# Kernel tuning notes

Measured on AMD Instinct MI355X. Metric: run time of the kernel, lower is better.

The kernel has to match this reference:

```python
import jax, jax.numpy as jnp
import numpy as np

NUM_HEADS = 16
DIM_EMBED = 1024
DIM_CROSS = 768
DIM_HEAD = DIM_EMBED // NUM_HEADS


def setup_inputs() -> dict:
    key = jax.random.key(0)
    ks = jax.random.split(key, 10)
    B, Sq, Skv = 16, 4096, 77
    s_e = 1.0 / np.sqrt(DIM_EMBED)
    s_c = 1.0 / np.sqrt(DIM_CROSS)
    return {
        "x": jax.random.normal(ks[0], (B, Sq, DIM_EMBED), jnp.float32),
        "y": jax.random.normal(ks[1], (B, Skv, DIM_CROSS), jnp.float32),
        "wq": jax.random.uniform(ks[2], (DIM_EMBED, DIM_EMBED), jnp.float32, -s_e, s_e),
        "bq": jax.random.uniform(ks[3], (DIM_EMBED,), jnp.float32, -s_e, s_e),
        "wk": jax.random.uniform(ks[4], (DIM_CROSS, DIM_EMBED), jnp.float32, -s_c, s_c),
        "bk": jax.random.uniform(ks[5], (DIM_EMBED,), jnp.float32, -s_c, s_c),
        "wv": jax.random.uniform(ks[6], (DIM_CROSS, DIM_EMBED), jnp.float32, -s_c, s_c),
        "bv": jax.random.uniform(ks[7], (DIM_EMBED,), jnp.float32, -s_c, s_c),
        "wo": jax.random.uniform(ks[8], (DIM_EMBED, DIM_EMBED), jnp.float32, -s_e, s_e),
        "bo": jax.random.uniform(ks[9], (DIM_EMBED,), jnp.float32, -s_e, s_e),
    }


def reference(x, y, wq, bq, wk, bk, wv, bv, wo, bo):
    B, Sq, E = x.shape
    H, D = NUM_HEADS, DIM_HEAD
    q = (x @ wq + bq).reshape(B, Sq, H, D).transpose(0, 2, 1, 3)   # [B,H,Sq,D]
    k = (y @ wk + bk).reshape(B, -1, H, D).transpose(0, 2, 1, 3)   # [B,H,Skv,D]
    v = (y @ wv + bv).reshape(B, -1, H, D).transpose(0, 2, 1, 3)   # [B,H,Skv,D]
    scale = 1.0 / jnp.sqrt(jnp.asarray(D, dtype=q.dtype))
    scores = jnp.einsum("bhqd,bhkd->bhqk", q, k) * scale           # [B,H,Sq,Skv]
    attn = jax.nn.softmax(scores, axis=-1)
    out = jnp.einsum("bhqk,bhkd->bhqd", attn, v)                   # [B,H,Sq,D]
    out = out.transpose(0, 2, 1, 3).reshape(B, Sq, E)
    return out @ wo + bo
```

## Files before the change

### kernel.cpp

```cpp
#include <hip/hip_runtime.h>

typedef unsigned short u16;
typedef __attribute__((ext_vector_type(4))) float f32x4;
typedef __attribute__((ext_vector_type(8))) short bf16x8;
typedef __attribute__((ext_vector_type(8))) unsigned short u16x8;
typedef __attribute__((ext_vector_type(4))) unsigned short u16x4;

__device__ __forceinline__ u16 f2bf(float f) {
  union { float f; unsigned u; } v; v.f = f;
  unsigned r = v.u + 0x7FFFu + ((v.u >> 16) & 1u);
  return (u16)(r >> 16);
}
__device__ __forceinline__ float bf2f(u16 h) {
  union { unsigned u; float f; } v; v.u = ((unsigned)h) << 16; return v.f;
}

__device__ __forceinline__ void gload_lds16(const void* g, void* l) {
  __builtin_amdgcn_global_load_lds((const __attribute__((address_space(1))) void*)g,
                                   (__attribute__((address_space(3))) void*)l, 16, 0, 0);
}


__global__ void k_zero(u16x8* __restrict__ p, int n8) {
  int i = blockIdx.x * blockDim.x + threadIdx.x;
  int stride = gridDim.x * blockDim.x;
  u16x8 z = (u16x8)0;
  for (; i < n8; i += stride) p[i] = z;
}

__global__ void k_cvt_x(const float* __restrict__ in, u16* __restrict__ out, int n4) {
  int i = blockIdx.x * blockDim.x + threadIdx.x;
  int stride = gridDim.x * blockDim.x;
  const f32x4* in4 = (const f32x4*)in;
  u16x4* out4 = (u16x4*)out;
  for (; i < n4; i += stride) {
    f32x4 v = in4[i];
    u16x4 o;
    o[0] = f2bf(v[0]); o[1] = f2bf(v[1]); o[2] = f2bf(v[2]); o[3] = f2bf(v[3]);
    out4[i] = o;
  }
}

__global__ void k_prep_wt(const float* __restrict__ wq, const float* __restrict__ wo,
                          const float* __restrict__ wk, const float* __restrict__ wv,
                          u16* __restrict__ WQ1T, u16* __restrict__ WO1T,
                          u16* __restrict__ WK1T, u16* __restrict__ WV1T) {
  __shared__ u16 tile[64][72];
  int bid = blockIdx.x;
  const float* w; u16* o; int K;
  if (bid < 256)      { w = wq; o = WQ1T; K = 1024; }
  else if (bid < 512) { w = wo; o = WO1T; K = 1024; bid -= 256; }
  else if (bid < 704) { w = wk; o = WK1T; K = 768;  bid -= 512; }
  else                { w = wv; o = WV1T; K = 768;  bid -= 704; }
  const int ti = bid >> 4, tj = bid & 15;
  const int t = threadIdx.x;
  const int r = t >> 2, cq = (t & 3) * 16;

  const float* src = w + (size_t)(ti * 64 + r) * 1024 + tj * 64 + cq;
#pragma unroll
  for (int j4 = 0; j4 < 4; ++j4) {
    f32x4 v = *(const f32x4*)(src + j4 * 4);
#pragma unroll
    for (int e = 0; e < 4; ++e) tile[r][cq + j4 * 4 + e] = f2bf(v[e]);
  }
  __syncthreads();

  u16 vals[16];
#pragma unroll
  for (int j = 0; j < 16; ++j) vals[j] = tile[cq + j][r];
  u16* dst = o + (size_t)(tj * 64 + r) * K + ti * 64 + cq;
  *(u16x8*)dst = *(u16x8*)&vals[0];
  *(u16x8*)(dst + 8) = *(u16x8*)&vals[8];
}

__global__ void k_prep_y(const float* __restrict__ y, u16* __restrict__ yb, int n4) {
  int i = blockIdx.x * blockDim.x + threadIdx.x;
  int stride = gridDim.x * blockDim.x;
  const f32x4* in4 = (const f32x4*)y;
  u16x4* out4 = (u16x4*)yb;
  for (; i < n4; i += stride) {
    f32x4 v = in4[i];
    u16x4 o;
    o[0] = f2bf(v[0]); o[1] = f2bf(v[1]); o[2] = f2bf(v[2]); o[3] = f2bf(v[3]);
    out4[i] = o;
  }
}

__global__ __launch_bounds__(256, 2) void k_gemm_kv(
    const u16* __restrict__ A,
    const u16* __restrict__ BK1, const float* __restrict__ bkb, u16* __restrict__ KTo,
    const u16* __restrict__ BV1, const float* __restrict__ bvb, u16* __restrict__ VTo)
{
  const int M = 1232, Kdim = 768;
  __shared__ u16 sA[128 * 32];
  __shared__ u16 sB[128 * 32];
  const int t = threadIdx.x;
  const int half = blockIdx.x >= 80;
  const int bb = blockIdx.x - half * 80;
  const u16* B = half ? BV1 : BK1;
  const float* bias = half ? bvb : bkb;
  u16* outp = half ? VTo : KTo;
  const int bm = bb / 8, bn = bb % 8;
  const int m0 = bm * 128, n0 = bn * 128;
  const int l = t & 63, wv_ = t >> 6;
  const int lr = l & 15, lg = l >> 4;
  const int wm = (wv_ >> 1) * 64, wn = (wv_ & 1) * 64;

  const int srow = t >> 2;
  const int ssw = ((t >> 2) & 3) ^ ((t >> 4) & 3);
  const int scol = ((t & 3) ^ ssw) * 8;
  char* ldsA = (char*)sA;
  char* ldsB = (char*)sB;
  const int ldsoff = wv_ * 1024;

  const int swl = (lr & 3) ^ ((lr >> 2) & 3);
  const int rds = (lg ^ swl) * 8;

  f32x4 acc[4][4] = {};

  for (int kt = 0; kt < Kdim / 32; ++kt) {
    const int k0 = kt * 32;
    __syncthreads();
    {
      int r1 = m0 + srow;       if (r1 > M - 1) r1 = M - 1;
      int r2 = m0 + 64 + srow;  if (r2 > M - 1) r2 = M - 1;
      gload_lds16(A + (size_t)r1 * Kdim + k0 + scol, ldsA + 0    + ldsoff);
      gload_lds16(A + (size_t)r2 * Kdim + k0 + scol, ldsA + 4096 + ldsoff);
      gload_lds16(B + (size_t)(n0 + srow) * Kdim + k0 + scol,      ldsB + 0    + ldsoff);
      gload_lds16(B + (size_t)(n0 + 64 + srow) * Kdim + k0 + scol, ldsB + 4096 + ldsoff);
    }
    __syncthreads();
    bf16x8 af[4], bfr[4];
#pragma unroll
    for (int mt = 0; mt < 4; ++mt)
      af[mt] = *(const bf16x8*)&sA[(wm + mt * 16 + lr) * 32 + rds];
#pragma unroll
    for (int nt = 0; nt < 4; ++nt)
      bfr[nt] = *(const bf16x8*)&sB[(wn + nt * 16 + lr) * 32 + rds];
#pragma unroll
    for (int mt = 0; mt < 4; ++mt)
#pragma unroll
      for (int nt = 0; nt < 4; ++nt)
        acc[mt][nt] = __builtin_amdgcn_mfma_f32_16x16x32_bf16(af[mt], bfr[nt], acc[mt][nt], 0, 0, 0);
  }

#pragma unroll
  for (int mt = 0; mt < 4; ++mt) {
#pragma unroll
    for (int nt = 0; nt < 4; ++nt) {
      const int gc = n0 + wn + nt * 16 + lr;
      const float bb2 = bias[gc];
#pragma unroll
      for (int r = 0; r < 4; ++r) {
        const int gr = m0 + wm + mt * 16 + lg * 4 + r;
        const float v = acc[mt][nt][r] + bb2;
        if (gr < M) {
          int bI = gr / 77, s = gr - bI * 77;
          int hh = gc >> 6, d = gc & 63;
          if (!half)
            outp[(((size_t)bI * 16 + hh) * 96 + s) * 64 + d] = f2bf(v);
          else
            outp[(((size_t)bI * 16 + hh) * 64 + d) * 96 + s] = f2bf(v);
        }
      }
    }
  }
}

template <int EPI>
__global__ __launch_bounds__(512, 2) void gemm256(
    const u16* __restrict__ A, const u16* __restrict__ Bp,
    const float* __restrict__ bias, void* __restrict__ outp)
{
  __shared__ char lds[131072];
  const int t = threadIdx.x;
  const int cpx = (int)gridDim.x >> 3;
  const int swz = ((int)blockIdx.x & 7) * cpx + ((int)blockIdx.x >> 3);
  const int bm = swz >> 2, bn = swz & 3;
  const int m0 = bm * 256, n0 = bn * 256;
  const int w = t >> 6, l = t & 63, lr = l & 15, lg = l >> 4;
  const int wm = w >> 2, wn = w & 3;

  const int srow = t >> 2;
  const int scol = ((t & 3) ^ ((t >> 2) & 3) ^ ((t >> 4) & 3)) * 8;
  const int rsw = (lg ^ (lr & 3) ^ ((lr >> 2) & 3)) << 4;
  const int arow = wm * 128 + lr;
  const int brow = wn * 64 + lr;

  f32x4 acc[8][4] = {};

#define RD(dstA, dstB, sbb) { \
  _Pragma("unroll") for (int q = 0; q < 8; ++q) \
    dstA[q] = *(const bf16x8*)(lds + (sbb) + ((arow + q * 16) << 6) + rsw); \
  _Pragma("unroll") for (int nt = 0; nt < 4; ++nt) \
    dstB[nt] = *(const bf16x8*)(lds + (sbb) + 16384 + ((brow + nt * 16) << 6) + rsw); }
#define STAGE(kt, sbb) { \
    gload_lds16(A  + (size_t)(m0 + srow) * 1024 + (kt) * 32 + scol,       lds + (sbb) + t * 16); \
    gload_lds16(A  + (size_t)(m0 + 128 + srow) * 1024 + (kt) * 32 + scol, lds + (sbb) + 8192 + t * 16); \
    gload_lds16(Bp + (size_t)(n0 + srow) * 1024 + (kt) * 32 + scol,       lds + (sbb) + 16384 + t * 16); \
    gload_lds16(Bp + (size_t)(n0 + 128 + srow) * 1024 + (kt) * 32 + scol, lds + (sbb) + 24576 + t * 16); }
#define MM(a_, b_) { __builtin_amdgcn_s_setprio(1); \
  _Pragma("unroll") for (int q = 0; q < 8; ++q) \
    _Pragma("unroll") for (int nt = 0; nt < 4; ++nt) \
      acc[q][nt] = __builtin_amdgcn_mfma_f32_16x16x32_bf16(a_[q], b_[nt], acc[q][nt], 0, 0, 0); \
  __builtin_amdgcn_s_setprio(0); }
#define BAR __builtin_amdgcn_s_barrier()
#define SB0 __builtin_amdgcn_sched_barrier(0)
#define VM8 asm volatile("s_waitcnt vmcnt(8)" ::: "memory")

  bf16x8 aA[8], bA[4], aB[8], bB[4];

  STAGE(0, 0); STAGE(1, 32768); STAGE(2, 65536);
  VM8; SB0; BAR;
  RD(aA, bA, 0);

  int rdo = 32768, sto = 98304;
#pragma unroll 1
  for (int tt = 0; tt < 32; tt += 2) {
    {
      int ks = tt + 3; if (ks > 31) ks = 31;
      STAGE(ks, sto); sto = (sto + 32768) & 131071;
      VM8; SB0; BAR;
      RD(aB, bB, rdo); rdo = (rdo + 32768) & 131071;
      MM(aA, bA);
      BAR;
    }
    {
      int ks = tt + 4; if (ks > 31) ks = 31;
      STAGE(ks, sto); sto = (sto + 32768) & 131071;
      VM8; SB0; BAR;
      RD(aA, bA, rdo); rdo = (rdo + 32768) & 131071;
      MM(aB, bB);
      BAR;
    }
  }
  asm volatile("s_waitcnt vmcnt(0)" ::: "memory");
  SB0;

#undef RD
#undef STAGE
#undef MM
#undef BAR
#undef SB0
#undef VM8

#pragma unroll
  for (int q = 0; q < 8; ++q) {
#pragma unroll
    for (int nt = 0; nt < 4; ++nt) {
      const int gc = n0 + wn * 64 + nt * 16 + lr;
      const float bb = bias[gc];
#pragma unroll
      for (int r = 0; r < 4; ++r) {
        const int gr = m0 + wm * 128 + q * 16 + lg * 4 + r;
        const float v = acc[q][nt][r] + bb;
        if constexpr (EPI == 0) {
          ((u16*)outp)[(size_t)gr * 1024 + gc] = f2bf(v);
        } else {
          ((float*)outp)[(size_t)gr * 1024 + gc] = v;
        }
      }
    }
  }
}

__global__ __launch_bounds__(256) void k_attn(const u16* __restrict__ KT,
                                              const u16* __restrict__ VT,
                                              u16* __restrict__ QB)
{
  __shared__ u16 sK[96 * 72];
  __shared__ u16 sV[64 * 104];
  __shared__ u16 sP[4][32 * 104];

  const int bid = blockIdx.x;
  const int h = bid & 15, b = (bid >> 4) & 15, blk = bid >> 8;
  const int t = threadIdx.x;

  const u16* gK = KT + (size_t)(b * 16 + h) * (96 * 64);
  const u16* gV = VT + (size_t)(b * 16 + h) * (64 * 96);
#pragma unroll
  for (int c = 0; c < 3; ++c) {
    int e = t * 8 + c * 2048;
    { int row = e >> 6, col = e & 63;
      *(u16x8*)&sK[row * 72 + col] = *(const u16x8*)&gK[e]; }
    { int row = e / 96, col = e - (e / 96) * 96;
      *(u16x8*)&sV[row * 104 + col] = *(const u16x8*)&gV[e]; }
  }
  __syncthreads();

  const int l = t & 63, w = t >> 6, lr = l & 15, lg = l >> 4;
  const size_t rowbase = (size_t)b * 4096 + blk * 128 + w * 32;

  bf16x8 aq[2][2];
#pragma unroll
  for (int mt = 0; mt < 2; ++mt)
#pragma unroll
    for (int ks = 0; ks < 2; ++ks)
      aq[mt][ks] = *(const bf16x8*)&QB[(rowbase + mt * 16 + lr) * 1024 + h * 64 + ks * 32 + lg * 8];

  f32x4 s_[2][5] = {};
#pragma unroll
  for (int nt = 0; nt < 5; ++nt) {
#pragma unroll
    for (int ks = 0; ks < 2; ++ks) {
      bf16x8 bk = *(const bf16x8*)&sK[(nt * 16 + lr) * 72 + ks * 32 + lg * 8];
#pragma unroll
      for (int mt = 0; mt < 2; ++mt)
        s_[mt][nt] = __builtin_amdgcn_mfma_f32_16x16x32_bf16(aq[mt][ks], bk, s_[mt][nt], 0, 0, 0);
    }
  }
#pragma unroll
  for (int mt = 0; mt < 2; ++mt)
#pragma unroll
    for (int nt = 0; nt < 5; ++nt)
#pragma unroll
      for (int r = 0; r < 4; ++r)
        s_[mt][nt][r] *= 0.125f;
  if (lr >= 13) {
#pragma unroll
    for (int mt = 0; mt < 2; ++mt)
#pragma unroll
      for (int r = 0; r < 4; ++r)
        s_[mt][4][r] = -1e30f;
  }

  float ri[2][4];
#pragma unroll
  for (int mt = 0; mt < 2; ++mt) {
#pragma unroll
    for (int r = 0; r < 4; ++r) {
      float m1 = s_[mt][0][r];
#pragma unroll
      for (int nt = 1; nt < 5; ++nt) m1 = fmaxf(m1, s_[mt][nt][r]);
      m1 = fmaxf(m1, __shfl_xor(m1, 1, 64));
      m1 = fmaxf(m1, __shfl_xor(m1, 2, 64));
      m1 = fmaxf(m1, __shfl_xor(m1, 4, 64));
      m1 = fmaxf(m1, __shfl_xor(m1, 8, 64));
      float s1 = 0.f;
#pragma unroll
      for (int nt = 0; nt < 5; ++nt) {
        float e = __expf(s_[mt][nt][r] - m1);
        s_[mt][nt][r] = e;
        s1 += e;
      }
      s1 += __shfl_xor(s1, 1, 64);
      s1 += __shfl_xor(s1, 2, 64);
      s1 += __shfl_xor(s1, 4, 64);
      s1 += __shfl_xor(s1, 8, 64);
      ri[mt][r] = 1.0f / s1;
    }
  }

#pragma unroll
  for (int mt = 0; mt < 2; ++mt)
#pragma unroll
    for (int nt = 0; nt < 5; ++nt)
#pragma unroll
      for (int r = 0; r < 4; ++r)
        sP[w][(mt * 16 + lg * 4 + r) * 104 + nt * 16 + lr] = f2bf(s_[mt][nt][r] * ri[mt][r]);
#pragma unroll
  for (int mt = 0; mt < 2; ++mt)
#pragma unroll
    for (int r = 0; r < 4; ++r)
      sP[w][(mt * 16 + lg * 4 + r) * 104 + 80 + lr] = 0;

  f32x4 o_[2][4] = {};
#pragma unroll
  for (int ks = 0; ks < 3; ++ks) {
    bf16x8 ap[2];
#pragma unroll
    for (int mt = 0; mt < 2; ++mt)
      ap[mt] = *(const bf16x8*)&sP[w][(mt * 16 + lr) * 104 + ks * 32 + lg * 8];
#pragma unroll
    for (int nt = 0; nt < 4; ++nt) {
      bf16x8 bv = *(const bf16x8*)&sV[(nt * 16 + lr) * 104 + ks * 32 + lg * 8];
#pragma unroll
      for (int mt = 0; mt < 2; ++mt)
        o_[mt][nt] = __builtin_amdgcn_mfma_f32_16x16x32_bf16(ap[mt], bv, o_[mt][nt], 0, 0, 0);
    }
  }

#pragma unroll
  for (int mt = 0; mt < 2; ++mt)
#pragma unroll
    for (int nt = 0; nt < 4; ++nt)
#pragma unroll
      for (int r = 0; r < 4; ++r)
        QB[(rowbase + mt * 16 + lg * 4 + r) * 1024 + h * 64 + nt * 16 + lr] = f2bf(o_[mt][nt][r]);
}


extern "C" void kernel_launch(void* const* d_in, const int* in_sizes, int n_in,
                              void* d_out, int out_size, void* d_ws, size_t ws_size,
                              hipStream_t stream) {
  const float* x  = (const float*)d_in[0];
  const float* y  = (const float*)d_in[1];
  const float* wq = (const float*)d_in[2];
  const float* bq = (const float*)d_in[3];
  const float* wk = (const float*)d_in[4];
  const float* bk = (const float*)d_in[5];
  const float* wv = (const float*)d_in[6];
  const float* bv = (const float*)d_in[7];
  const float* wo = (const float*)d_in[8];
  const float* bo = (const float*)d_in[9];

  char* ws = (char*)d_ws;
  u16* QB   = (u16*)(ws + 0);
  u16* WQ1T = (u16*)(ws + 134217728);
  u16* WO1T = (u16*)(ws + 136314880);
  u16* WK1T = (u16*)(ws + 138412032);
  u16* WV1T = (u16*)(ws + 139984896);
  u16* YB   = (u16*)(ws + 141557760);
  u16* KT   = (u16*)(ws + 143654912);
  u16* VT   = (u16*)(ws + 146800640);

  u16*   XB  = (u16*)d_out;
  float* OUT = (float*)d_out;

  k_zero<<<768, 256, 0, stream>>>((u16x8*)KT, 393216);
  k_cvt_x<<<4096, 256, 0, stream>>>(x, XB, 16777216);
  k_prep_wt<<<896, 256, 0, stream>>>(wq, wo, wk, wv, WQ1T, WO1T, WK1T, WV1T);
  k_prep_y<<<924, 256, 0, stream>>>(y, YB, 236544);

  k_gemm_kv<<<160, 256, 0, stream>>>(YB, WK1T, bk, KT, WV1T, bv, VT);

  gemm256<0><<<1024, 512, 0, stream>>>(XB, WQ1T, bq, QB);

  k_attn<<<8192, 256, 0, stream>>>(KT, VT, QB);

  gemm256<1><<<1024, 512, 0, stream>>>(QB, WO1T, bo, OUT);
}
```

Before: 531.5 us.

## Fuse attention into the Q-projection GEMM epilogue

Removes the separate attention kernel. The Q-projection GEMM epilogue now stages each warp's Q tile (one head, 32-row chunks) in LDS, computes scores, softmax and P·V against K/V read directly from global memory, and writes the attention output instead of Q. This avoids writing Q to memory and reading it back in a second launch. In exchange, K and V fragments are loaded from global or L2 with no LDS staging, and the GEMM epilogue becomes much longer, which may affect register pressure under launch_bounds(512,2).

```diff
diff --git a/kernel.cpp b/kernel.cpp
--- a/kernel.cpp
+++ b/kernel.cpp
@@ -170,7 +170,8 @@
 template <int EPI>
 __global__ __launch_bounds__(512, 2) void gemm256(
     const u16* __restrict__ A, const u16* __restrict__ Bp,
-    const float* __restrict__ bias, void* __restrict__ outp)
+    const float* __restrict__ bias, void* __restrict__ outp,
+    const u16* __restrict__ KT, const u16* __restrict__ VT)
 {
   __shared__ char lds[131072];
   const int t = threadIdx.x;
@@ -235,7 +236,7 @@
     }
   }
   asm volatile("s_waitcnt vmcnt(0)" ::: "memory");
-  SB0;
+  SB0; BAR;
 
 #undef RD
 #undef STAGE
@@ -244,149 +245,143 @@
 #undef SB0
 #undef VM8
 
-#pragma unroll
-  for (int q = 0; q < 8; ++q) {
-#pragma unroll
-    for (int nt = 0; nt < 4; ++nt) {
-      const int gc = n0 + wn * 64 + nt * 16 + lr;
-      const float bb = bias[gc];
-#pragma unroll
-      for (int r = 0; r < 4; ++r) {
-        const int gr = m0 + wm * 128 + q * 16 + lg * 4 + r;
-        const float v = acc[q][nt][r] + bb;
-        if constexpr (EPI == 0) {
-          ((u16*)outp)[(size_t)gr * 1024 + gc] = f2bf(v);
-        } else {
-          ((float*)outp)[(size_t)gr * 1024 + gc] = v;
+  if constexpr (EPI == 1) {
+#pragma unroll
+    for (int q = 0; q < 8; ++q) {
+#pragma unroll
+      for (int nt = 0; nt < 4; ++nt) {
+        const int gc = n0 + wn * 64 + nt * 16 + lr;
+        const float bb = bias[gc];
+#pragma unroll
+        for (int r = 0; r < 4; ++r) {
+          const int gr = m0 + wm * 128 + q * 16 + lg * 4 + r;
+          ((float*)outp)[(size_t)gr * 1024 + gc] = acc[q][nt][r] + bb;
         }
       }
     }
-  }
-}
-
-__global__ __launch_bounds__(256) void k_attn(const u16* __restrict__ KT,
-                                              const u16* __restrict__ VT,
-                                              u16* __restrict__ QB)
-{
-  __shared__ u16 sK[96 * 72];
-  __shared__ u16 sV[64 * 104];
-  __shared__ u16 sP[4][32 * 104];
-
-  const int bid = blockIdx.x;
-  const int h = bid & 15, b = (bid >> 4) & 15, blk = bid >> 8;
-  const int t = threadIdx.x;
-
-  const u16* gK = KT + (size_t)(b * 16 + h) * (96 * 64);
-  const u16* gV = VT + (size_t)(b * 16 + h) * (64 * 96);
-#pragma unroll
-  for (int c = 0; c < 3; ++c) {
-    int e = t * 8 + c * 2048;
-    { int row = e >> 6, col = e & 63;
-      *(u16x8*)&sK[row * 72 + col] = *(const u16x8*)&gK[e]; }
-    { int row = e / 96, col = e - (e / 96) * 96;
-      *(u16x8*)&sV[row * 104 + col] = *(const u16x8*)&gV[e]; }
-  }
-  __syncthreads();
-
-  const int l = t & 63, w = t >> 6, lr = l & 15, lg = l >> 4;
-  const size_t rowbase = (size_t)b * 4096 + blk * 128 + w * 32;
-
-  bf16x8 aq[2][2];
-#pragma unroll
-  for (int mt = 0; mt < 2; ++mt)
-#pragma unroll
-    for (int ks = 0; ks < 2; ++ks)
-      aq[mt][ks] = *(const bf16x8*)&QB[(rowbase + mt * 16 + lr) * 1024 + h * 64 + ks * 32 + lg * 8];
-
-  f32x4 s_[2][5] = {};
-#pragma unroll
-  for (int nt = 0; nt < 5; ++nt) {
-#pragma unroll
-    for (int ks = 0; ks < 2; ++ks) {
-      bf16x8 bk = *(const bf16x8*)&sK[(nt * 16 + lr) * 72 + ks * 32 + lg * 8];
-#pragma unroll
-      for (int mt = 0; mt < 2; ++mt)
-        s_[mt][nt] = __builtin_amdgcn_mfma_f32_16x16x32_bf16(aq[mt][ks], bk, s_[mt][nt], 0, 0, 0);
-    }
-  }
-#pragma unroll
-  for (int mt = 0; mt < 2; ++mt)
-#pragma unroll
-    for (int nt = 0; nt < 5; ++nt)
-#pragma unroll
-      for (int r = 0; r < 4; ++r)
-        s_[mt][nt][r] *= 0.125f;
-  if (lr >= 13) {
-#pragma unroll
-    for (int mt = 0; mt < 2; ++mt)
-#pragma unroll
-      for (int r = 0; r < 4; ++r)
-        s_[mt][4][r] = -1e30f;
-  }
-
-  float ri[2][4];
-#pragma unroll
-  for (int mt = 0; mt < 2; ++mt) {
-#pragma unroll
-    for (int r = 0; r < 4; ++r) {
-      float m1 = s_[mt][0][r];
-#pragma unroll
-      for (int nt = 1; nt < 5; ++nt) m1 = fmaxf(m1, s_[mt][nt][r]);
-      m1 = fmaxf(m1, __shfl_xor(m1, 1, 64));
-      m1 = fmaxf(m1, __shfl_xor(m1, 2, 64));
-      m1 = fmaxf(m1, __shfl_xor(m1, 4, 64));
-      m1 = fmaxf(m1, __shfl_xor(m1, 8, 64));
-      float s1 = 0.f;
+  } else {
+    const int hh = (n0 >> 6) + wn;
+    const int b = m0 >> 12;
+    const u16* gK = KT + (size_t)(b * 16 + hh) * (96 * 64);
+    const u16* gV = VT + (size_t)(b * 16 + hh) * (64 * 96);
+    u16* Qs = (u16*)(lds + w * 16384);
+    u16* Ps = (u16*)(lds + w * 16384 + 8192);
+    u16* QBo = (u16*)outp;
+
+    float bb[4];
+#pragma unroll
+    for (int nt = 0; nt < 4; ++nt) bb[nt] = bias[n0 + wn * 64 + nt * 16 + lr];
+
+#pragma unroll
+    for (int cc = 0; cc < 4; ++cc) {
+#pragma unroll
+      for (int qq = 0; qq < 2; ++qq)
+#pragma unroll
+        for (int nt = 0; nt < 4; ++nt)
+#pragma unroll
+          for (int r = 0; r < 4; ++r)
+            Qs[(qq * 16 + lg * 4 + r) * 72 + nt * 16 + lr] =
+                f2bf(acc[cc * 2 + qq][nt][r] + bb[nt]);
+
+      bf16x8 aq[2][2];
+#pragma unroll
+      for (int qq = 0; qq < 2; ++qq)
+#pragma unroll
+        for (int ks = 0; ks < 2; ++ks)
+          aq[qq][ks] = *(const bf16x8*)&Qs[(qq * 16 + lr) * 72 + ks * 32 + lg * 8];
+
+      f32x4 s_[2][5] = {};
 #pragma unroll
       for (int nt = 0; nt < 5; ++nt) {
-        float e = __expf(s_[mt][nt][r] - m1);
-        s_[mt][nt][r] = e;
-        s1 += e;
-      }
-      s1 += __shfl_xor(s1, 1, 64);
-      s1 += __shfl_xor(s1, 2, 64);
-      s1 += __shfl_xor(s1, 4, 64);
-      s1 += __shfl_xor(s1, 8, 64);
-      ri[mt][r] = 1.0f / s1;
-    }
-  }
-
-#pragma unroll
-  for (int mt = 0; mt < 2; ++mt)
-#pragma unroll
-    for (int nt = 0; nt < 5; ++nt)
-#pragma unroll
-      for (int r = 0; r < 4; ++r)
-        sP[w][(mt * 16 + lg * 4 + r) * 104 + nt * 16 + lr] = f2bf(s_[mt][nt][r] * ri[mt][r]);
-#pragma unroll
-  for (int mt = 0; mt < 2; ++mt)
-#pragma unroll
-    for (int r = 0; r < 4; ++r)
-      sP[w][(mt * 16 + lg * 4 + r) * 104 + 80 + lr] = 0;
-
-  f32x4 o_[2][4] = {};
-#pragma unroll
-  for (int ks = 0; ks < 3; ++ks) {
-    bf16x8 ap[2];
-#pragma unroll
-    for (int mt = 0; mt < 2; ++mt)
-      ap[mt] = *(const bf16x8*)&sP[w][(mt * 16 + lr) * 104 + ks * 32 + lg * 8];
-#pragma unroll
-    for (int nt = 0; nt < 4; ++nt) {
-      bf16x8 bv = *(const bf16x8*)&sV[(nt * 16 + lr) * 104 + ks * 32 + lg * 8];
-#pragma unroll
-      for (int mt = 0; mt < 2; ++mt)
-        o_[mt][nt] = __builtin_amdgcn_mfma_f32_16x16x32_bf16(ap[mt], bv, o_[mt][nt], 0, 0, 0);
-    }
-  }
-
-#pragma unroll
-  for (int mt = 0; mt < 2; ++mt)
-#pragma unroll
-    for (int nt = 0; nt < 4; ++nt)
-#pragma unroll
-      for (int r = 0; r < 4; ++r)
-        QB[(rowbase + mt * 16 + lg * 4 + r) * 1024 + h * 64 + nt * 16 + lr] = f2bf(o_[mt][nt][r]);
+#pragma unroll
+        for (int ks = 0; ks < 2; ++ks) {
+          bf16x8 bk = *(const bf16x8*)&gK[(nt * 16 + lr) * 64 + ks * 32 + lg * 8];
+#pragma unroll
+          for (int qq = 0; qq < 2; ++qq)
+            s_[qq][nt] = __builtin_amdgcn_mfma_f32_16x16x32_bf16(aq[qq][ks], bk, s_[qq][nt], 0, 0, 0);
+        }
+      }
+#pragma unroll
+      for (int qq = 0; qq < 2; ++qq)
+#pragma unroll
+        for (int nt = 0; nt < 5; ++nt)
+#pragma unroll
+          for (int r = 0; r < 4; ++r)
+            s_[qq][nt][r] *= 0.125f;
+      if (lr >= 13) {
+#pragma unroll
+        for (int qq = 0; qq < 2; ++qq)
+#pragma unroll
+          for (int r = 0; r < 4; ++r)
+            s_[qq][4][r] = -1e30f;
+      }
+
+      float ri[2][4];
+#pragma unroll
+      for (int qq = 0; qq < 2; ++qq) {
+#pragma unroll
+        for (int r = 0; r < 4; ++r) {
+          float m1 = s_[qq][0][r];
+#pragma unroll
+          for (int nt = 1; nt < 5; ++nt) m1 = fmaxf(m1, s_[qq][nt][r]);
+          m1 = fmaxf(m1, __shfl_xor(m1, 1, 64));
+          m1 = fmaxf(m1, __shfl_xor(m1, 2, 64));
+          m1 = fmaxf(m1, __shfl_xor(m1, 4, 64));
+          m1 = fmaxf(m1, __shfl_xor(m1, 8, 64));
+          float s1 = 0.f;
+#pragma unroll
+          for (int nt = 0; nt < 5; ++nt) {
+            float e = __expf(s_[qq][nt][r] - m1);
+            s_[qq][nt][r] = e;
+            s1 += e;
+          }
+          s1 += __shfl_xor(s1, 1, 64);
+          s1 += __shfl_xor(s1, 2, 64);
+          s1 += __shfl_xor(s1, 4, 64);
+          s1 += __shfl_xor(s1, 8, 64);
+          ri[qq][r] = 1.0f / s1;
+        }
+      }
+
+#pragma unroll
+      for (int qq = 0; qq < 2; ++qq)
+#pragma unroll
+        for (int nt = 0; nt < 5; ++nt)
+#pragma unroll
+          for (int r = 0; r < 4; ++r)
+            Ps[(qq * 16 + lg * 4 + r) * 104 + nt * 16 + lr] = f2bf(s_[qq][nt][r] * ri[qq][r]);
+#pragma unroll
+      for (int qq = 0; qq < 2; ++qq)
+#pragma unroll
+        for (int r = 0; r < 4; ++r)
+          Ps[(qq * 16 + lg * 4 + r) * 104 + 80 + lr] = 0;
+
+      f32x4 o_[2][4] = {};
+#pragma unroll
+      for (int ks = 0; ks < 3; ++ks) {
+        bf16x8 ap[2];
+#pragma unroll
+        for (int qq = 0; qq < 2; ++qq)
+          ap[qq] = *(const bf16x8*)&Ps[(qq * 16 + lr) * 104 + ks * 32 + lg * 8];
+#pragma unroll
+        for (int nt = 0; nt < 4; ++nt) {
+          bf16x8 bv = *(const bf16x8*)&gV[(nt * 16 + lr) * 96 + ks * 32 + lg * 8];
+#pragma unroll
+          for (int qq = 0; qq < 2; ++qq)
+            o_[qq][nt] = __builtin_amdgcn_mfma_f32_16x16x32_bf16(ap[qq], bv, o_[qq][nt], 0, 0, 0);
+        }
+      }
+
+#pragma unroll
+      for (int qq = 0; qq < 2; ++qq)
+#pragma unroll
+        for (int nt = 0; nt < 4; ++nt)
+#pragma unroll
+          for (int r = 0; r < 4; ++r)
+            QBo[(size_t)(m0 + wm * 128 + cc * 32 + qq * 16 + lg * 4 + r) * 1024
+                + hh * 64 + nt * 16 + lr] = f2bf(o_[qq][nt][r]);
+    }
+  }
 }
 
 
@@ -424,9 +419,7 @@
 
   k_gemm_kv<<<160, 256, 0, stream>>>(YB, WK1T, bk, KT, WV1T, bv, VT);
 
-  gemm256<0><<<1024, 512, 0, stream>>>(XB, WQ1T, bq, QB);
-
-  k_attn<<<8192, 256, 0, stream>>>(KT, VT, QB);
-
-  gemm256<1><<<1024, 512, 0, stream>>>(QB, WO1T, bo, OUT);
-}
+  gemm256<0><<<1024, 512, 0, stream>>>(XB, WQ1T, bq, QB, KT, VT);
+
+  gemm256<1><<<1024, 512, 0, stream>>>(QB, WO1T, bo, OUT, nullptr, nullptr);
+}
```

Measured after the change: 533.6 us. About the same (+0.4%).
